# Performance work log

Hardware: AMD Instinct MI355X
Metric: run time of the kernel (lower is better)

## Reference

```python
import jax, jax.numpy as jnp
import numpy as np

D_MODEL = 1024
HEADS = 16
D_K = D_MODEL // HEADS


def setup_inputs() -> dict:
    key = jax.random.key(0)
    ks = jax.random.split(key, 11)
    B, S = 4, 2048
    scale = 1.0 / np.sqrt(D_MODEL)
    return {
        "q": jax.random.normal(ks[0], (B, S, D_MODEL), jnp.float32),
        "k": jax.random.normal(ks[1], (B, S, D_MODEL), jnp.float32),
        "v": jax.random.normal(ks[2], (B, S, D_MODEL), jnp.float32),
        "wq": jax.random.normal(ks[3], (D_MODEL, D_MODEL), jnp.float32) * scale,
        "bq": jax.random.normal(ks[4], (D_MODEL,), jnp.float32) * 0.01,
        "wk": jax.random.normal(ks[5], (D_MODEL, D_MODEL), jnp.float32) * scale,
        "bk": jax.random.normal(ks[6], (D_MODEL,), jnp.float32) * 0.01,
        "wv": jax.random.normal(ks[7], (D_MODEL, D_MODEL), jnp.float32) * scale,
        "bv": jax.random.normal(ks[8], (D_MODEL,), jnp.float32) * 0.01,
        "wo": jax.random.normal(ks[9], (D_MODEL, D_MODEL), jnp.float32) * scale,
        "bo": jax.random.normal(ks[10], (D_MODEL,), jnp.float32) * 0.01,
    }


def reference(q, k, v, wq, bq, wk, bk, wv, bv, wo, bo):
    B, S, _ = q.shape
    # nn.Linear: x @ W^T + b
    qp = q @ wq.T + bq
    kp = k @ wk.T + bk
    vp = v @ wv.T + bv
    # [B, S, D] -> [B, H, S, d_k]
    def split_heads(x):
        return x.reshape(B, S, HEADS, D_K).transpose(0, 2, 1, 3)
    qh, kh, vh = split_heads(qp), split_heads(kp), split_heads(vp)
    # scaled dot-product attention (dropout p=0 -> identity)
    scores = jnp.einsum("bhsd,bhtd->bhst", qh, kh) / jnp.sqrt(jnp.float32(D_K)).astype(qh.dtype)
    attn = jax.nn.softmax(scores, axis=-1)
    ctx = jnp.einsum("bhst,bhtd->bhsd", attn, vh)
    # merge heads and output projection
    ctx = ctx.transpose(0, 2, 1, 3).reshape(B, S, D_MODEL)
    return ctx @ wo.T + bo
```

## Files before the change

kernel.cpp:

```cpp
#include <hip/hip_runtime.h>


typedef __attribute__((ext_vector_type(8))) short bf16x8;
typedef __attribute__((ext_vector_type(4))) float f32x4;
typedef unsigned int u32;

#define DEVI __device__ __forceinline__

static constexpr int S_LEN = 2048;
static constexpr int NH = 16;
static constexpr int DK = 64;
static constexpr float Q_SCALE = 0.125f * 1.44269504088896340736f;

DEVI unsigned short f2b(float f) {
    unsigned int u = __builtin_bit_cast(unsigned int, f);
    u += 0x7fffu + ((u >> 16) & 1u);
    return (unsigned short)(u >> 16);
}

DEVI u32 pkbf16(float a, float b) {
#if __has_builtin(__builtin_amdgcn_cvt_pk_bf16_f32)
    auto r = __builtin_amdgcn_cvt_pk_bf16_f32(a, b);
    return __builtin_bit_cast(u32, r);
#else
    return (u32)f2b(a) | ((u32)f2b(b) << 16);
#endif
}

DEVI f32x4 mfma16(bf16x8 a, bf16x8 b, f32x4 c) {
    return __builtin_amdgcn_mfma_f32_16x16x32_bf16(a, b, c, 0, 0, 0);
}

#define GLL16(g, l)                                                        \
    __builtin_amdgcn_global_load_lds(                                      \
        (const __attribute__((address_space(1))) u32*)(g),                 \
        (__attribute__((address_space(3))) u32*)(l), 16, 0, 0)

__global__ __launch_bounds__(256) void cvt3(
    const float* __restrict__ q, const float* __restrict__ k,
    const float* __restrict__ v, unsigned short* __restrict__ dq,
    unsigned short* __restrict__ dk, unsigned short* __restrict__ dv) {
    const int z = blockIdx.y;
    const float* src = z == 0 ? q : z == 1 ? k : v;
    unsigned short* dst = z == 0 ? dq : z == 1 ? dk : dv;
    long i = ((long)blockIdx.x * 256 + threadIdx.x) * 8;
    float4 v0 = *(const float4*)(src + i);
    float4 v1 = *(const float4*)(src + i + 4);
    uint4 o;
    o.x = pkbf16(v0.x, v0.y);
    o.y = pkbf16(v0.z, v0.w);
    o.z = pkbf16(v1.x, v1.y);
    o.w = pkbf16(v1.z, v1.w);
    *(uint4*)(dst + i) = o;
}

__global__ __launch_bounds__(256) void cvt_w(
    const float* __restrict__ a, const float* __restrict__ b,
    const float* __restrict__ c, const float* __restrict__ d,
    unsigned short* __restrict__ o) {
    const float* src = blockIdx.y == 0 ? a : blockIdx.y == 1 ? b
                     : blockIdx.y == 2 ? c : d;
    unsigned short* dst = o + (long)blockIdx.y * 1048576;
    long i = ((long)blockIdx.x * 256 + threadIdx.x) * 8;
    float4 v0 = *(const float4*)(src + i);
    float4 v1 = *(const float4*)(src + i + 4);
    uint4 ov;
    ov.x = pkbf16(v0.x, v0.y);
    ov.y = pkbf16(v0.z, v0.w);
    ov.z = pkbf16(v1.x, v1.y);
    ov.w = pkbf16(v1.z, v1.w);
    *(uint4*)(dst + i) = ov;
}

__global__ __launch_bounds__(256) void gemm_qkv(
    const unsigned short* __restrict__ aq, const unsigned short* __restrict__ ak,
    const unsigned short* __restrict__ av, const unsigned short* __restrict__ wqkv,
    const float* __restrict__ bq, const float* __restrict__ bk,
    const float* __restrict__ bv, unsigned short* __restrict__ qh,
    unsigned short* __restrict__ kh, unsigned short* __restrict__ vht) {
    __shared__ __align__(16) unsigned short As[2][128 * 32];
    __shared__ __align__(16) unsigned short Bs[2][128 * 32];
    const int tid = threadIdx.x;
    const int w = tid >> 6, l = tid & 63, l16 = l & 15, quad = l >> 4;
    const int wm = (w >> 1) * 64, wn = (w & 1) * 64;
    const int m0 = blockIdx.y * 128, n0 = blockIdx.x * 128;
    const int z = blockIdx.z;
    const unsigned short* A = z == 0 ? aq : z == 1 ? ak : av;
    const unsigned short* W = wqkv + (long)z * 1048576;
    const float* bias = z == 0 ? bq : z == 1 ? bk : bv;

    f32x4 acc[4][4] = {};

    auto stage = [&](int kt, int buf) {
        #pragma unroll
        for (int h = 0; h < 2; ++h) {
            int sb = h * 256 + w * 64;
            int slot = sb + l;
            int row = slot >> 2, c = (slot & 3) ^ ((row >> 1) & 3);
            GLL16(A + (long)(m0 + row) * 1024 + kt + c * 8, &As[buf][sb * 8]);
            GLL16(W + (long)(n0 + row) * 1024 + kt + c * 8, &Bs[buf][sb * 8]);
        }
    };

    stage(0, 0);
    __syncthreads();

    for (int ki = 0; ki < 32; ++ki) {
        if (ki < 31) stage((ki + 1) * 32, (ki + 1) & 1);
        const unsigned short* as = As[ki & 1];
        const unsigned short* bs = Bs[ki & 1];
        bf16x8 a[4], b[4];
        #pragma unroll
        for (int i = 0; i < 4; ++i) {
            int r = wm + i * 16 + l16;
            a[i] = *(const bf16x8*)(as + (r * 4 + (quad ^ ((r >> 1) & 3))) * 8);
        }
        #pragma unroll
        for (int j = 0; j < 4; ++j) {
            int r = wn + j * 16 + l16;
            b[j] = *(const bf16x8*)(bs + (r * 4 + (quad ^ ((r >> 1) & 3))) * 8);
        }
        #pragma unroll
        for (int i = 0; i < 4; ++i)
            #pragma unroll
            for (int j = 0; j < 4; ++j)
                acc[i][j] = mfma16(a[i], b[j], acc[i][j]);
        __syncthreads();
    }

    if (z < 2) {
        unsigned short* out = z == 0 ? qh : kh;
        const float scale = z == 0 ? Q_SCALE : 1.0f;
        #pragma unroll
        for (int j = 0; j < 4; ++j) {
            int n = n0 + wn + j * 16 + l16;
            float bvl = bias[n];
            int hh = n >> 6, dd = n & 63;
            #pragma unroll
            for (int i = 0; i < 4; ++i)
                #pragma unroll
                for (int r = 0; r < 4; ++r) {
                    int m = m0 + wm + i * 16 + quad * 4 + r;
                    int bb = m >> 11, ss = m & 2047;
                    out[(((long)(bb * NH + hh) * S_LEN + ss) * DK) + dd] =
                        f2b((acc[i][j][r] + bvl) * scale);
                }
        }
    } else {
        unsigned short* out = vht;
        #pragma unroll
        for (int j = 0; j < 4; ++j) {
            int n = n0 + wn + j * 16 + l16;
            float bvl = bias[n];
            int hh = n >> 6, dd = n & 63;
            #pragma unroll
            for (int i = 0; i < 4; ++i) {
                int m = m0 + wm + i * 16 + quad * 4;
                int bb = m >> 11, ss = m & 2047;
                uint2 pk;
                pk.x = pkbf16(acc[i][j][0] + bvl, acc[i][j][1] + bvl);
                pk.y = pkbf16(acc[i][j][2] + bvl, acc[i][j][3] + bvl);
                *(uint2*)(out + ((long)(bb * NH + hh) * DK + dd) * S_LEN + ss) = pk;
            }
        }
    }
}

__global__ __launch_bounds__(256) void gemm_out(
    const unsigned short* __restrict__ A, const unsigned short* __restrict__ W,
    const float* __restrict__ bias, float* __restrict__ out) {
    __shared__ __align__(16) unsigned short As[2][128 * 32];
    __shared__ __align__(16) unsigned short Bs[2][128 * 32];
    const int tid = threadIdx.x;
    const int w = tid >> 6, l = tid & 63, l16 = l & 15, quad = l >> 4;
    const int wm = (w >> 1) * 64, wn = (w & 1) * 64;
    const int m0 = blockIdx.y * 128, n0 = blockIdx.x * 128;

    f32x4 acc[4][4] = {};

    auto stage = [&](int kt, int buf) {
        #pragma unroll
        for (int h = 0; h < 2; ++h) {
            int sb = h * 256 + w * 64;
            int slot = sb + l;
            int row = slot >> 2, c = (slot & 3) ^ ((row >> 1) & 3);
            GLL16(A + (long)(m0 + row) * 1024 + kt + c * 8, &As[buf][sb * 8]);
            GLL16(W + (long)(n0 + row) * 1024 + kt + c * 8, &Bs[buf][sb * 8]);
        }
    };

    stage(0, 0);
    __syncthreads();

    for (int ki = 0; ki < 32; ++ki) {
        if (ki < 31) stage((ki + 1) * 32, (ki + 1) & 1);
        const unsigned short* as = As[ki & 1];
        const unsigned short* bs = Bs[ki & 1];
        bf16x8 a[4], b[4];
        #pragma unroll
        for (int i = 0; i < 4; ++i) {
            int r = wm + i * 16 + l16;
            a[i] = *(const bf16x8*)(as + (r * 4 + (quad ^ ((r >> 1) & 3))) * 8);
        }
        #pragma unroll
        for (int j = 0; j < 4; ++j) {
            int r = wn + j * 16 + l16;
            b[j] = *(const bf16x8*)(bs + (r * 4 + (quad ^ ((r >> 1) & 3))) * 8);
        }
        #pragma unroll
        for (int i = 0; i < 4; ++i)
            #pragma unroll
            for (int j = 0; j < 4; ++j)
                acc[i][j] = mfma16(a[i], b[j], acc[i][j]);
        __syncthreads();
    }

    #pragma unroll
    for (int j = 0; j < 4; ++j) {
        int n = n0 + wn + j * 16 + l16;
        float bv = bias[n];
        #pragma unroll
        for (int i = 0; i < 4; ++i)
            #pragma unroll
            for (int r = 0; r < 4; ++r) {
                int m = m0 + wm + i * 16 + quad * 4 + r;
                out[(long)m * 1024 + n] = acc[i][j][r] + bv;
            }
    }
}

__global__ __launch_bounds__(256, 4) void attn(
    const unsigned short* __restrict__ qh, const unsigned short* __restrict__ kh,
    const unsigned short* __restrict__ vht, unsigned short* __restrict__ ctx) {
    __shared__ __align__(16) unsigned short Kb[2][4096];
    __shared__ __align__(16) unsigned short Vb[4096];
    __shared__ __align__(16) unsigned short P[128 * 44];

    const int id = blockIdx.y * 16 + blockIdx.x;
    const int id2 = (id & 7) * 128 + (id >> 3);
    const int qt = id2 & 15, bh = id2 >> 4;
    const int tid = threadIdx.x;
    const int w = tid >> 6, l = tid & 63, l16 = l & 15, quad = l >> 4;

    const unsigned short* kh_b = kh + (long)bh * 2048 * 64;
    const unsigned short* vh_b = vht + (long)bh * 64 * 2048;

    const unsigned short* qsrc = qh + ((long)bh * 2048 + qt * 128) * 64;
    bf16x8 qf[2][2];
    #pragma unroll
    for (int dd = 0; dd < 2; ++dd)
        #pragma unroll
        for (int i = 0; i < 2; ++i)
            qf[dd][i] = *(const bf16x8*)(qsrc + (w * 32 + i * 16 + l16) * 64 +
                                         dd * 32 + quad * 8);

    auto stage_k = [&](const unsigned short* base, int buf) {
        #pragma unroll
        for (int rr = 0; rr < 2; ++rr) {
            int sb = rr * 256 + w * 64;
            int slot = sb + l;
            int row = slot >> 3, cc = (slot & 7) ^ (row & 7);
            GLL16(base + (long)row * 64 + cc * 8, &Kb[buf][sb * 8]);
        }
    };
    auto stage_v = [&](const unsigned short* vbase) {
        #pragma unroll
        for (int rr = 0; rr < 2; ++rr) {
            int sb = rr * 256 + w * 64;
            int slot = sb + l;
            int d = slot >> 3, cc = (slot & 7) ^ (d & 7);
            GLL16(vbase + (long)d * 2048 + cc * 8, &Vb[sb * 8]);
        }
    };

    stage_k(kh_b, 0);
    __syncthreads();

    f32x4 o[4][2] = {};
    float lsum[2] = {0.f, 0.f};

    for (int kt = 0; kt < 32; ++kt) {
        if (kt < 31) stage_k(kh_b + (long)(kt + 1) * 64 * 64, (kt + 1) & 1);
        stage_v(vh_b + kt * 64);

        const unsigned short* kb = Kb[kt & 1];
        f32x4 sa[2][4] = {};
        #pragma unroll
        for (int dd = 0; dd < 2; ++dd) {
            bf16x8 kf[4];
            #pragma unroll
            for (int ja = 0; ja < 4; ++ja) {
                int row = ja * 16 + l16;
                kf[ja] = *(const bf16x8*)(kb + (row * 8 + ((dd * 4 + quad) ^ (row & 7))) * 8);
            }
            #pragma unroll
            for (int i = 0; i < 2; ++i)
                #pragma unroll
                for (int ja = 0; ja < 4; ++ja)
                    sa[i][ja] = mfma16(kf[ja], qf[dd][i], sa[i][ja]);
        }

        #pragma unroll
        for (int i = 0; i < 2; ++i)
            #pragma unroll
            for (int ja = 0; ja < 4; ++ja)
                #pragma unroll
                for (int r = 0; r < 4; ++r) {
                    float p = exp2f(sa[i][ja][r]);
                    sa[i][ja][r] = p;
                    lsum[i] += p;
                }

        __syncthreads();

        #pragma unroll
        for (int qtr = 0; qtr < 2; ++qtr) {
            #pragma unroll
            for (int jh = 0; jh < 2; ++jh)
                #pragma unroll
                for (int i = 0; i < 2; ++i) {
                    int row = w * 32 + i * 16 + l16;
                    int ja = qtr * 2 + jh;
                    uint2 pk;
                    pk.x = pkbf16(sa[i][ja][0], sa[i][ja][1]);
                    pk.y = pkbf16(sa[i][ja][2], sa[i][ja][3]);
                    *(uint2*)(&P[row * 44 + jh * 16 + quad * 4]) = pk;
                }
            bf16x8 vf[4], pf[2];
            #pragma unroll
            for (int jd = 0; jd < 4; ++jd) {
                int d = jd * 16 + l16;
                vf[jd] = *(const bf16x8*)(Vb + (d * 8 + ((qtr * 4 + quad) ^ (d & 7))) * 8);
            }
            #pragma unroll
            for (int i = 0; i < 2; ++i) {
                int row = w * 32 + i * 16 + l16;
                pf[i] = *(const bf16x8*)(&P[row * 44 + quad * 8]);
            }
            #pragma unroll
            for (int jd = 0; jd < 4; ++jd)
                #pragma unroll
                for (int i = 0; i < 2; ++i)
                    o[jd][i] = mfma16(vf[jd], pf[i], o[jd][i]);
        }
        __syncthreads();
    }

    #pragma unroll
    for (int i = 0; i < 2; ++i) {
        lsum[i] += __shfl_xor(lsum[i], 16);
        lsum[i] += __shfl_xor(lsum[i], 32);
    }

    const int b = bh >> 4, hh = bh & 15;
    #pragma unroll
    for (int i = 0; i < 2; ++i) {
        float inv = 1.0f / lsum[i];
        int s = qt * 128 + w * 32 + i * 16 + l16;
        #pragma unroll
        for (int jd = 0; jd < 4; ++jd) {
            uint2 pk;
            pk.x = pkbf16(o[jd][i][0] * inv, o[jd][i][1] * inv);
            pk.y = pkbf16(o[jd][i][2] * inv, o[jd][i][3] * inv);
            *(uint2*)(&ctx[((long)(b * 2048 + s) * 1024) + hh * 64 + jd * 16 + quad * 4]) = pk;
        }
    }
}

extern "C" void kernel_launch(void* const* d_in, const int* in_sizes, int n_in,
                              void* d_out, int out_size, void* d_ws, size_t ws_size,
                              hipStream_t stream) {
    const float* q  = (const float*)d_in[0];
    const float* k  = (const float*)d_in[1];
    const float* v  = (const float*)d_in[2];
    const float* wq = (const float*)d_in[3];
    const float* bq = (const float*)d_in[4];
    const float* wk = (const float*)d_in[5];
    const float* bk = (const float*)d_in[6];
    const float* wv = (const float*)d_in[7];
    const float* bv = (const float*)d_in[8];
    const float* wo = (const float*)d_in[9];
    const float* bo = (const float*)d_in[10];
    float* out = (float*)d_out;

    const size_t NE = 8u * 1024u * 1024u;
    unsigned short* ab_q = (unsigned short*)d_ws;
    unsigned short* qh   = ab_q + NE;
    unsigned short* kh   = qh + NE;
    unsigned short* vht  = kh + NE;
    unsigned short* wb   = vht + NE;
    unsigned short* wob  = wb + 3 * 1048576;
    unsigned short* ctx  = ab_q;
    unsigned short* ab_k = (unsigned short*)d_out;
    unsigned short* ab_v = ab_k + NE;

    dim3 blk(256);
    cvt_w<<<dim3(512, 4), blk, 0, stream>>>(wq, wk, wv, wo, wb);
    cvt3<<<dim3(4096, 3), blk, 0, stream>>>(q, k, v, ab_q, ab_k, ab_v);
    gemm_qkv<<<dim3(8, 64, 3), blk, 0, stream>>>(ab_q, ab_k, ab_v, wb,
                                                 bq, bk, bv, qh, kh, vht);
    attn<<<dim3(16, 64), blk, 0, stream>>>(qh, kh, vht, ctx);
    gemm_out<<<dim3(8, 64), blk, 0, stream>>>(ctx, wob, bo, out);
}
```

Baseline: 406.8 us.

## Triple-buffer V tiles, drop trailing barrier, compute softmax row sums via MFMA

V tiles are now triple-buffered and prefetched one iteration ahead alongside K, so V loads overlap compute instead of being issued in the same iteration they are used. The barrier at the end of each key-tile iteration is removed; the mid-iteration barrier plus the extra buffering is relied on to keep shared-memory reuse safe. Softmax row sums are accumulated with an extra MFMA against an all-ones bf16 operand instead of scalar adds and final shuffles, so the sums now come from bf16-rounded probabilities. exp2 uses the hardware builtin, and the occupancy hint is lowered to 3 blocks per CU to make room for the larger LDS footprint.

Result: faster. 376.2 us (-7.5%).

```diff
diff --git a/kernel.cpp b/kernel.cpp
--- a/kernel.cpp
+++ b/kernel.cpp
@@ -24,6 +24,14 @@
     return __builtin_bit_cast(u32, r);
 #else
     return (u32)f2b(a) | ((u32)f2b(b) << 16);
+#endif
+}
+
+DEVI float fexp2(float x) {
+#if __has_builtin(__builtin_amdgcn_exp2f)
+    return __builtin_amdgcn_exp2f(x);
+#else
+    return exp2f(x);
 #endif
 }
 
@@ -229,11 +237,11 @@
     }
 }
 
-__global__ __launch_bounds__(256, 4) void attn(
+__global__ __launch_bounds__(256, 3) void attn(
     const unsigned short* __restrict__ qh, const unsigned short* __restrict__ kh,
     const unsigned short* __restrict__ vht, unsigned short* __restrict__ ctx) {
     __shared__ __align__(16) unsigned short Kb[2][4096];
-    __shared__ __align__(16) unsigned short Vb[4096];
+    __shared__ __align__(16) unsigned short Vb[3][4096];
     __shared__ __align__(16) unsigned short P[128 * 44];
 
     const int id = blockIdx.y * 16 + blockIdx.x;
@@ -263,25 +271,32 @@
             GLL16(base + (long)row * 64 + cc * 8, &Kb[buf][sb * 8]);
         }
     };
-    auto stage_v = [&](const unsigned short* vbase) {
+    auto stage_v = [&](const unsigned short* vbase, int buf) {
         #pragma unroll
         for (int rr = 0; rr < 2; ++rr) {
             int sb = rr * 256 + w * 64;
             int slot = sb + l;
             int d = slot >> 3, cc = (slot & 7) ^ (d & 7);
-            GLL16(vbase + (long)d * 2048 + cc * 8, &Vb[sb * 8]);
+            GLL16(vbase + (long)d * 2048 + cc * 8, &Vb[buf][sb * 8]);
         }
     };
 
     stage_k(kh_b, 0);
+    stage_v(vh_b, 0);
     __syncthreads();
 
     f32x4 o[4][2] = {};
-    float lsum[2] = {0.f, 0.f};
-
+    f32x4 osum[2] = {};
+    bf16x8 ones;
+    #pragma unroll
+    for (int j = 0; j < 8; ++j) ones[j] = (short)0x3f80;
+
+    int vs = 1, vr = 0;
     for (int kt = 0; kt < 32; ++kt) {
-        if (kt < 31) stage_k(kh_b + (long)(kt + 1) * 64 * 64, (kt + 1) & 1);
-        stage_v(vh_b + kt * 64);
+        if (kt < 31) {
+            stage_k(kh_b + (long)(kt + 1) * 64 * 64, (kt + 1) & 1);
+            stage_v(vh_b + (kt + 1) * 64, vs);
+        }
 
         const unsigned short* kb = Kb[kt & 1];
         f32x4 sa[2][4] = {};
@@ -305,14 +320,12 @@
             #pragma unroll
             for (int ja = 0; ja < 4; ++ja)
                 #pragma unroll
-                for (int r = 0; r < 4; ++r) {
-                    float p = exp2f(sa[i][ja][r]);
-                    sa[i][ja][r] = p;
-                    lsum[i] += p;
-                }
+                for (int r = 0; r < 4; ++r)
+                    sa[i][ja][r] = fexp2(sa[i][ja][r]);
 
         __syncthreads();
 
+        const unsigned short* vb = Vb[vr];
         #pragma unroll
         for (int qtr = 0; qtr < 2; ++qtr) {
             #pragma unroll
@@ -330,7 +343,7 @@
             #pragma unroll
             for (int jd = 0; jd < 4; ++jd) {
                 int d = jd * 16 + l16;
-                vf[jd] = *(const bf16x8*)(Vb + (d * 8 + ((qtr * 4 + quad) ^ (d & 7))) * 8);
+                vf[jd] = *(const bf16x8*)(vb + (d * 8 + ((qtr * 4 + quad) ^ (d & 7))) * 8);
             }
             #pragma unroll
             for (int i = 0; i < 2; ++i) {
@@ -342,20 +355,19 @@
                 #pragma unroll
                 for (int i = 0; i < 2; ++i)
                     o[jd][i] = mfma16(vf[jd], pf[i], o[jd][i]);
-        }
-        __syncthreads();
-    }
-
-    #pragma unroll
-    for (int i = 0; i < 2; ++i) {
-        lsum[i] += __shfl_xor(lsum[i], 16);
-        lsum[i] += __shfl_xor(lsum[i], 32);
+            #pragma unroll
+            for (int i = 0; i < 2; ++i)
+                osum[i] = mfma16(ones, pf[i], osum[i]);
+        }
+
+        vr = (vr + 1 == 3) ? 0 : vr + 1;
+        vs = (vs + 1 == 3) ? 0 : vs + 1;
     }
 
     const int b = bh >> 4, hh = bh & 15;
     #pragma unroll
     for (int i = 0; i < 2; ++i) {
-        float inv = 1.0f / lsum[i];
+        float inv = 1.0f / osum[i][0];
         int s = qt * 128 + w * 32 + i * 16 + l16;
         #pragma unroll
         for (int jd = 0; jd < 4; ++jd) {
```
